# Kernel tuning notes

Hardware: AMD Instinct MI355X
Metric: run time of the kernel (lower is better)

## Reference

```python
import jax, jax.numpy as jnp
import numpy as np

B, L, C, V = 16, 600, 256, 256
OUT_SEQ = 6000
KSZ = 5
DILATIONS = (1, 2, 4)
N_BLOCKS = 10
COND = 256  # speaker(128) + noise(128)
TEMP = 10.0
EPS = 1e-5


def _ccbn(x, cond, gw, gb, bw, bb):
    # x: (B, C, L); conditional batch-norm: per-channel stats over (batch, length),
    # gamma/beta predicted from condition vector.
    mu = jnp.mean(x, axis=(0, 2), keepdims=True)
    var = jnp.var(x, axis=(0, 2), keepdims=True)
    xn = (x - mu) * jax.lax.rsqrt(var + EPS)
    gamma = 1.0 + cond @ gw + gb  # (B, C)
    beta = cond @ bw + bb         # (B, C)
    return xn * gamma[:, :, None] + beta[:, :, None]


def _conv1d(x, w, b, dil=1):
    # x: (B, C_in, L); w: (C_out, C_in, K)
    y = jax.lax.conv_general_dilated(
        x, w, window_strides=(1,), padding='SAME', rhs_dilation=(dil,),
        dimension_numbers=('NCH', 'OIH', 'NCH'))
    return y + b[None, :, None]


def setup_inputs() -> dict:
    key = jax.random.key(0)
    ks = jax.random.split(key, 20)
    s = 0.02
    inp = {
        'inputs': jax.random.randint(ks[0], (B, L), 0, V),
        'speaker_embeddings': jax.random.normal(ks[1], (B, 128), jnp.float32),
        'noise': jax.random.normal(ks[2], (B, 128), jnp.float32),
        'emb': jax.random.normal(ks[3], (V, C), jnp.float32) * s,
        # 10 blocks x 3 dilated convs
        'conv_w': jax.random.normal(ks[4], (N_BLOCKS, 3, C, C, KSZ), jnp.float32) * s,
        'conv_b': jnp.zeros((N_BLOCKS, 3, C), jnp.float32),
        # CCBN projections per conv (gamma/beta from condition)
        'g_w': jax.random.normal(ks[5], (N_BLOCKS, 3, COND, C), jnp.float32) * s,
        'g_b': jnp.zeros((N_BLOCKS, 3, C), jnp.float32),
        'b_w': jax.random.normal(ks[6], (N_BLOCKS, 3, COND, C), jnp.float32) * s,
        'b_b': jnp.zeros((N_BLOCKS, 3, C), jnp.float32),
        # TokenLength head: 2 CCBNs + conv1 (256->256,k1) + conv2 (256->1,k1)
        'tl_g_w': jax.random.normal(ks[7], (2, COND, C), jnp.float32) * s,
        'tl_g_b': jnp.zeros((2, C), jnp.float32),
        'tl_b_w': jax.random.normal(ks[8], (2, COND, C), jnp.float32) * s,
        'tl_b_b': jnp.zeros((2, C), jnp.float32),
        'tl_conv1_w': jax.random.normal(ks[9], (C, C, 1), jnp.float32) * s,
        'tl_conv1_b': jnp.zeros((C,), jnp.float32),
        'tl_conv2_w': jax.random.normal(ks[10], (1, C, 1), jnp.float32) * s,
        'tl_conv2_b': jnp.zeros((1,), jnp.float32),
    }
    return inp


def reference(inputs, speaker_embeddings, noise, emb, conv_w, conv_b,
              g_w, g_b, b_w, b_b, tl_g_w, tl_g_b, tl_b_w, tl_b_b,
              tl_conv1_w, tl_conv1_b, tl_conv2_w, tl_conv2_b):
    cond = jnp.concatenate([speaker_embeddings, noise], axis=-1)  # (B, COND)
    x = emb[inputs]                    # (B, L, C)
    x = jnp.transpose(x, (0, 2, 1))    # (B, C, L)

    # 10 unaligned blocks: residual stacks of CCBN -> ReLU -> dilated conv
    for blk in range(N_BLOCKS):
        y = x
        for j, d in enumerate(DILATIONS):
            y = jax.nn.relu(_ccbn(y, cond, g_w[blk, j], g_b[blk, j], b_w[blk, j], b_b[blk, j]))
            y = _conv1d(y, conv_w[blk, j], conv_b[blk, j], dil=d)
        x = x + y
    unaligned = x  # (B, C, L)

    # TokenLength head
    t = jax.nn.relu(_ccbn(unaligned, cond, tl_g_w[0], tl_g_b[0], tl_b_w[0], tl_b_b[0]))
    t = _conv1d(t, tl_conv1_w, tl_conv1_b)
    t = jax.nn.relu(_ccbn(t, cond, tl_g_w[1], tl_g_b[1], tl_b_w[1], tl_b_b[1]))
    t = _conv1d(t, tl_conv2_w, tl_conv2_b)  # (B, 1, L)
    token_lengths = jax.nn.relu(t[:, 0, :])  # (B, L)

    token_ends = jnp.cumsum(token_lengths, axis=-1)        # (B, L)
    token_centers = token_ends - token_lengths / 2.0        # (B, L)
    aligned_lengths = token_ends

    out_pos = jnp.arange(OUT_SEQ, dtype=jnp.float32)         # (OUT,)
    diff = token_centers[:, None, :] - out_pos[None, :, None]  # (B, OUT, L)
    logits = -(diff * diff) / TEMP
    weights = jax.nn.softmax(logits, axis=-1)                # (B, OUT, L)

    feats = jnp.transpose(unaligned, (0, 2, 1))              # (B, L, C)
    aligned_features = jnp.einsum('bol,blc->boc', weights, feats)  # (B, OUT, C)
    return aligned_features, aligned_lengths
```

## Files before the change

### kernel.cpp

```cpp
#include <hip/hip_runtime.h>
#include <math.h>

#define EPSv 1e-5f

typedef short short8 __attribute__((ext_vector_type(8)));
typedef float floatx4 __attribute__((ext_vector_type(4)));

__device__ __forceinline__ unsigned short f2bf(float x) {
  unsigned u = __float_as_uint(x);
  unsigned r = (u + 0x7fffu + ((u >> 16) & 1u)) >> 16;
  return (unsigned short)r;
}

__global__ void k_zero(float* __restrict__ p) {
  p[blockIdx.x * 256 + threadIdx.x] = 0.f;
}

__global__ void k_gamma_beta(const float* __restrict__ spk, const float* __restrict__ noise,
                             const float* __restrict__ g_w, const float* __restrict__ g_b,
                             const float* __restrict__ b_w, const float* __restrict__ b_b,
                             const float* __restrict__ tl_g_w, const float* __restrict__ tl_g_b,
                             const float* __restrict__ tl_b_w, const float* __restrict__ tl_b_b,
                             float* __restrict__ gammas, float* __restrict__ betas) {
  __shared__ float condl[16*256];
  int t = threadIdx.x;
  for (int idx = t; idx < 4096; idx += 256) {
    int b = idx >> 8, k = idx & 255;
    condl[idx] = (k < 128) ? spk[b*128 + k] : noise[b*128 + k - 128];
  }
  __syncthreads();
  int i = blockIdx.x;
  const float *gw, *bw, *gbias, *bbias;
  if (i < 30) { gw = g_w + (size_t)i*65536; bw = b_w + (size_t)i*65536; gbias = g_b + i*256; bbias = b_b + i*256; }
  else { int j = i - 30; gw = tl_g_w + (size_t)j*65536; bw = tl_b_w + (size_t)j*65536; gbias = tl_g_b + j*256; bbias = tl_b_b + j*256; }
  int co = (t & 63) + blockIdx.y * 64;
  int slot = t >> 6;
  float g[4] = {0.f,0.f,0.f,0.f}, bt[4] = {0.f,0.f,0.f,0.f};
  for (int k = 0; k < 256; ++k) {
    float gwv = gw[k*256 + co];
    float bwv = bw[k*256 + co];
    #pragma unroll
    for (int bb = 0; bb < 4; ++bb) {
      float cv = condl[(slot*4 + bb)*256 + k];
      g[bb]  = fmaf(cv, gwv, g[bb]);
      bt[bb] = fmaf(cv, bwv, bt[bb]);
    }
  }
  #pragma unroll
  for (int bb = 0; bb < 4; ++bb) {
    int b = slot*4 + bb;
    gammas[i*4096 + b*256 + co] = 1.0f + g[bb] + gbias[co];
    betas [i*4096 + b*256 + co] = bt[bb] + bbias[co];
  }
}

template<int TAPS>
__device__ __forceinline__ void wprep_body(const float* __restrict__ src,
                                           unsigned short* __restrict__ dst,
                                           int cotile, int chunk, int t) {
  int cow = t >> 2, ci8 = (t & 3) * 8;
  const float* s0 = src + ((size_t)(cotile*64 + cow)*256 + chunk*32 + ci8)*TAPS;
  float v[8*TAPS];
  #pragma unroll
  for (int i = 0; i < 8*TAPS; ++i) v[i] = s0[i];
  unsigned short* dblk = dst + (size_t)cotile*(8*TAPS*4096) + (size_t)chunk*(TAPS*4096);
  #pragma unroll
  for (int tap = 0; tap < TAPS; ++tap) {
    unsigned hi2[4], lo2[4];
    #pragma unroll
    for (int jj = 0; jj < 4; ++jj) {
      float a = v[(jj*2+0)*TAPS + tap], b = v[(jj*2+1)*TAPS + tap];
      unsigned short ha = f2bf(a), hb = f2bf(b);
      unsigned short la = f2bf(a - __uint_as_float((unsigned)ha << 16));
      unsigned short lb = f2bf(b - __uint_as_float((unsigned)hb << 16));
      hi2[jj] = (unsigned)ha | ((unsigned)hb << 16);
      lo2[jj] = (unsigned)la | ((unsigned)lb << 16);
    }
    uint4 H; H.x = hi2[0]; H.y = hi2[1]; H.z = hi2[2]; H.w = hi2[3];
    uint4 L; L.x = lo2[0]; L.y = lo2[1]; L.z = lo2[2]; L.w = lo2[3];
    *(uint4*)(dblk + (size_t)(tap*2)*2048 + cow*32 + ci8) = H;
    *(uint4*)(dblk + (size_t)(tap*2+1)*2048 + cow*32 + ci8) = L;
  }
}

__global__ __launch_bounds__(256) void k_wprep(const float* __restrict__ conv_w,
                                               const float* __restrict__ tl_c1_w,
                                               unsigned short* __restrict__ wp) {
  int cc = blockIdx.x;
  int cotile = blockIdx.y >> 3, chunk = blockIdx.y & 7;
  if (cc == 30) wprep_body<1>(tl_c1_w, wp + (size_t)30*655360, cotile, chunk, threadIdx.x);
  else          wprep_body<5>(conv_w + (size_t)cc*327680, wp + (size_t)cc*655360, cotile, chunk, threadIdx.x);
}

__global__ void k_embed2(const int* __restrict__ inp, const float* __restrict__ emb,
                         float* __restrict__ x, float* __restrict__ stat0) {
  int bx = blockIdx.x;
  int c = threadIdx.x;
  int r0 = bx * 60;
  float s = 0.f, s2 = 0.f;
  for (int r = 0; r < 60; ++r) {
    int row = inp[r0 + r];
    float v = emb[(size_t)row*256 + c];
    x[(size_t)(r0 + r)*256 + c] = v;
    s += v; s2 = fmaf(v, v, s2);
  }
  atomicAdd(&stat0[c], s);
  atomicAdd(&stat0[256 + c], s2);
}

template<int TAPS>
__global__ __launch_bounds__(256) void k_convm(const float* __restrict__ zin, float* __restrict__ out,
                        const float* __restrict__ stat_in, float* __restrict__ stat_out,
                        const float* __restrict__ gam, const float* __restrict__ bet,
                        const unsigned short* __restrict__ wpc,
                        const float* __restrict__ bias, int dil, int mode) {
  __shared__ unsigned short Zhi[80*40];
  __shared__ unsigned short Zlo[80*40];
  __shared__ float s_sc[256];
  __shared__ float s_sh[256];
  __shared__ float lsum[64];
  __shared__ float lsq[64];
  int t = threadIdx.x;
  int bx = blockIdx.x;
  int b  = bx / 10;
  int l0 = (bx % 10) * 64;
  int co0 = blockIdx.y * 64;
  int PAD = ((TAPS - 1)/2) * dil;
  int ROWS = 64 + 2*PAD;
  int w = t >> 6, lane = t & 63;
  int lsub = (w & 1) * 32, cosub = (w >> 1) * 32;
  int quad = lane >> 4, nlan = lane & 15;
  if (t < 64) { lsum[t] = 0.f; lsq[t] = 0.f; }
  {
    float s = stat_in[t], s2 = stat_in[256 + t];
    float mu = s * (1.0f/9600.0f);
    float var = s2 * (1.0f/9600.0f) - mu*mu;
    float rs = rsqrtf(var + EPSv);
    float scale = rs * gam[b*256 + t];
    s_sc[t] = scale;
    s_sh[t] = fmaf(-mu, scale, bet[b*256 + t]);
  }

  floatx4 acc[2][2];
  #pragma unroll
  for (int i = 0; i < 2; ++i)
    #pragma unroll
    for (int j = 0; j < 2; ++j) acc[i][j] = (floatx4){0.f,0.f,0.f,0.f};

  const float* zb = zin + (size_t)b*600*256;
  int srow = t >> 3, fq = t & 7;
  int ar0 = (lsub + nlan) * 40 + quad * 8;
  int ar1 = (lsub + 16 + nlan) * 40 + quad * 8;

  for (int chunk = 0; chunk < 8; ++chunk) {
    int ci0 = chunk * 32;
    const unsigned short* pch = wpc + (size_t)(blockIdx.y*8 + chunk) * (TAPS*4096);
    short8 bh[TAPS][2], bl[TAPS][2];
    #pragma unroll
    for (int tap = 0; tap < TAPS; ++tap) {
      #pragma unroll
      for (int nt = 0; nt < 2; ++nt) {
        int cw = (cosub + nt*16 + nlan)*32 + quad*8;
        bh[tap][nt] = *(const short8*)(pch + (size_t)(tap*2)*2048 + cw);
        bl[tap][nt] = *(const short8*)(pch + (size_t)(tap*2+1)*2048 + cw);
      }
    }
    __syncthreads();
    float4 sc4 = *(const float4*)&s_sc[ci0 + fq*4];
    float4 sh4 = *(const float4*)&s_sh[ci0 + fq*4];
    for (int r = srow; r < ROWS; r += 32) {
      int gl = l0 - PAD + r;
      bool inr = (gl >= 0 && gl < 600);
      float4 z = {0,0,0,0};
      if (inr) z = *(const float4*)&zb[(size_t)gl*256 + ci0 + fq*4];
      float v0 = inr ? fmaxf(fmaf(z.x, sc4.x, sh4.x), 0.f) : 0.f;
      float v1 = inr ? fmaxf(fmaf(z.y, sc4.y, sh4.y), 0.f) : 0.f;
      float v2 = inr ? fmaxf(fmaf(z.z, sc4.z, sh4.z), 0.f) : 0.f;
      float v3 = inr ? fmaxf(fmaf(z.w, sc4.w, sh4.w), 0.f) : 0.f;
      unsigned short h0 = f2bf(v0), h1 = f2bf(v1), h2 = f2bf(v2), h3 = f2bf(v3);
      unsigned short e0 = f2bf(v0 - __uint_as_float((unsigned)h0 << 16));
      unsigned short e1 = f2bf(v1 - __uint_as_float((unsigned)h1 << 16));
      unsigned short e2 = f2bf(v2 - __uint_as_float((unsigned)h2 << 16));
      unsigned short e3 = f2bf(v3 - __uint_as_float((unsigned)h3 << 16));
      uint2 vh; vh.x = (unsigned)h0 | ((unsigned)h1 << 16);
      vh.y = (unsigned)h2 | ((unsigned)h3 << 16);
      uint2 vl; vl.x = (unsigned)e0 | ((unsigned)e1 << 16);
      vl.y = (unsigned)e2 | ((unsigned)e3 << 16);
      *(uint2*)&Zhi[r*40 + fq*4] = vh;
      *(uint2*)&Zlo[r*40 + fq*4] = vl;
    }
    __syncthreads();
    #pragma unroll
    for (int tap = 0; tap < TAPS; ++tap) {
      int sh = tap * dil * 40;
      short8 ah0 = *(const short8*)&Zhi[ar0 + sh];
      short8 ah1 = *(const short8*)&Zhi[ar1 + sh];
      short8 al0 = *(const short8*)&Zlo[ar0 + sh];
      short8 al1 = *(const short8*)&Zlo[ar1 + sh];
      #pragma unroll
      for (int nt = 0; nt < 2; ++nt) {
        acc[0][nt] = __builtin_amdgcn_mfma_f32_16x16x32_bf16(ah0, bh[tap][nt], acc[0][nt], 0, 0, 0);
        acc[0][nt] = __builtin_amdgcn_mfma_f32_16x16x32_bf16(ah0, bl[tap][nt], acc[0][nt], 0, 0, 0);
        acc[0][nt] = __builtin_amdgcn_mfma_f32_16x16x32_bf16(al0, bh[tap][nt], acc[0][nt], 0, 0, 0);
        acc[1][nt] = __builtin_amdgcn_mfma_f32_16x16x32_bf16(ah1, bh[tap][nt], acc[1][nt], 0, 0, 0);
        acc[1][nt] = __builtin_amdgcn_mfma_f32_16x16x32_bf16(ah1, bl[tap][nt], acc[1][nt], 0, 0, 0);
        acc[1][nt] = __builtin_amdgcn_mfma_f32_16x16x32_bf16(al1, bh[tap][nt], acc[1][nt], 0, 0, 0);
      }
    }
  }

  float bsv[2], ssum[2] = {0.f, 0.f}, ssq[2] = {0.f, 0.f};
  #pragma unroll
  for (int nt = 0; nt < 2; ++nt) bsv[nt] = bias[co0 + cosub + nt*16 + nlan];
  #pragma unroll
  for (int mt = 0; mt < 2; ++mt) {
    #pragma unroll
    for (int r = 0; r < 4; ++r) {
      int l = l0 + lsub + mt*16 + quad*4 + r;
      if (l < 600) {
        size_t rowo = ((size_t)(b*600 + l))*256 + co0 + cosub;
        #pragma unroll
        for (int nt = 0; nt < 2; ++nt) {
          float v = acc[mt][nt][r] + bsv[nt];
          float* dst = &out[rowo + nt*16 + nlan];
          if (mode) v += *dst;
          *dst = v;
          ssum[nt] += v;
          ssq[nt] = fmaf(v, v, ssq[nt]);
        }
      }
    }
  }
  #pragma unroll
  for (int nt = 0; nt < 2; ++nt) {
    ssum[nt] += __shfl_xor(ssum[nt], 16, 64);
    ssum[nt] += __shfl_xor(ssum[nt], 32, 64);
    ssq[nt]  += __shfl_xor(ssq[nt], 16, 64);
    ssq[nt]  += __shfl_xor(ssq[nt], 32, 64);
  }
  if (quad == 0) {
    #pragma unroll
    for (int nt = 0; nt < 2; ++nt) {
      atomicAdd(&lsum[cosub + nt*16 + nlan], ssum[nt]);
      atomicAdd(&lsq [cosub + nt*16 + nlan], ssq[nt]);
    }
  }
  __syncthreads();
  if (t < 64) {
    atomicAdd(&stat_out[co0 + t], lsum[t]);
    atomicAdd(&stat_out[256 + co0 + t], lsq[t]);
  }
}

__global__ void k_tl2(const float* __restrict__ z, const float* __restrict__ stat,
                      const float* __restrict__ gam, const float* __restrict__ bet,
                      const float* __restrict__ w2, const float* __restrict__ b2,
                      float* __restrict__ tl) {
  int t = threadIdx.x;
  int row = blockIdx.x * 4 + (t >> 6);
  int lane = t & 63;
  int b = row / 600;
  float4 s1 = *(const float4*)&stat[lane*4];
  float4 s2 = *(const float4*)&stat[256 + lane*4];
  float4 gm = *(const float4*)&gam[b*256 + lane*4];
  float4 bt = *(const float4*)&bet[b*256 + lane*4];
  float sc[4], sh[4];
  {
    float sv[4] = {s1.x, s1.y, s1.z, s1.w};
    float qv[4] = {s2.x, s2.y, s2.z, s2.w};
    float gv[4] = {gm.x, gm.y, gm.z, gm.w};
    float bv[4] = {bt.x, bt.y, bt.z, bt.w};
    #pragma unroll
    for (int i = 0; i < 4; ++i) {
      float mu = sv[i] * (1.0f/9600.0f);
      float var = qv[i] * (1.0f/9600.0f) - mu*mu;
      float rs = rsqrtf(var + EPSv);
      sc[i] = rs * gv[i];
      sh[i] = fmaf(-mu, sc[i], bv[i]);
    }
  }
  float4 zr = *(const float4*)&z[(size_t)row*256 + lane*4];
  float4 wr = *(const float4*)&w2[lane*4];
  float z0 = fmaxf(fmaf(zr.x, sc[0], sh[0]), 0.f);
  float z1 = fmaxf(fmaf(zr.y, sc[1], sh[1]), 0.f);
  float z2 = fmaxf(fmaf(zr.z, sc[2], sh[2]), 0.f);
  float z3 = fmaxf(fmaf(zr.w, sc[3], sh[3]), 0.f);
  float s = z0*wr.x + z1*wr.y + z2*wr.z + z3*wr.w;
  for (int m = 32; m >= 1; m >>= 1) s += __shfl_xor(s, m, 64);
  if (lane == 0) tl[row] = fmaxf(s + b2[0], 0.f);
}

__global__ void k_cumsum(const float* __restrict__ tl, float* __restrict__ centers,
                         float* __restrict__ out_len) {
  int b = blockIdx.x; int lane = threadIdx.x;
  float carry = 0.f;
  for (int ch = 0; ch < 10; ++ch) {
    int l = ch*64 + lane;
    float v = (l < 600) ? tl[b*600 + l] : 0.f;
    float s = v;
    #pragma unroll
    for (int off = 1; off < 64; off <<= 1) {
      float n = __shfl_up(s, off, 64);
      if (lane >= off) s += n;
    }
    float ends = carry + s;
    if (l < 600) {
      centers[b*600 + l] = ends - 0.5f*v;
      out_len[b*600 + l] = ends;
    }
    carry = __shfl(ends, 63, 64);
  }
}

__global__ void k_tobf16(const float* __restrict__ x, unsigned short* __restrict__ fbT) {
  __shared__ unsigned short T[64*66];
  int b = blockIdx.x, lt = blockIdx.y, ct = blockIdx.z;
  int t = threadIdx.x;
  int i4 = t >> 6;
  int j = t & 63;
  #pragma unroll
  for (int r = 0; r < 16; ++r) {
    int li = i4*16 + r;
    int l = lt*64 + li;
    float v = (l < 600) ? x[((size_t)(b*600 + l))*256 + ct*64 + j] : 0.f;
    T[j*66 + li] = f2bf(v);
  }
  __syncthreads();
  int row = t >> 2, seg = (t & 3) * 16;
  unsigned vv[8];
  #pragma unroll
  for (int k = 0; k < 8; ++k)
    vv[k] = *(const unsigned*)&T[row*66 + seg + k*2];
  size_t dsth = ((size_t)(b*256 + ct*64 + row))*640 + lt*64 + seg;
  unsigned* du = (unsigned*)fbT;
  uint4 a; a.x = vv[0]; a.y = vv[1]; a.z = vv[2]; a.w = vv[3];
  uint4 c4; c4.x = vv[4]; c4.y = vv[5]; c4.z = vv[6]; c4.w = vv[7];
  *(uint4*)(du + dsth/2) = a;
  *(uint4*)(du + dsth/2 + 4) = c4;
}

__global__ __launch_bounds__(256) void k_align2(const unsigned short* __restrict__ fbT,
                        const float* __restrict__ centers, float* __restrict__ outp) {
  __shared__ float cen[600];
  __shared__ float mrow[64];
  __shared__ float isum[64];
  __shared__ unsigned short Wt[64*72];
  __shared__ unsigned short Ft[256*72];
  int b = blockIdx.x;
  int o0 = blockIdx.y * 64;
  int t = threadIdx.x;
  int wv = t >> 6, lane = t & 63;
  for (int i = t; i < 600; i += 256) cen[i] = centers[b*600 + i];
  __syncthreads();
  for (int rr = 0; rr < 16; ++rr) {
    int oi = wv*16 + rr;
    float opos = (float)(o0 + oi);
    float mx = -3.0e38f;
    for (int l = lane; l < 600; l += 64) {
      float d = cen[l] - opos;
      mx = fmaxf(mx, -d*d*0.1f);
    }
    #pragma unroll
    for (int mm = 32; mm >= 1; mm >>= 1) mx = fmaxf(mx, __shfl_xor(mx, mm, 64));
    float sum = 0.f;
    for (int l = lane; l < 600; l += 64) {
      float d = cen[l] - opos;
      sum += __expf(-d*d*0.1f - mx);
    }
    #pragma unroll
    for (int mm = 32; mm >= 1; mm >>= 1) sum += __shfl_xor(sum, mm, 64);
    if (lane == 0) { mrow[oi] = mx; isum[oi] = 1.0f / sum; }
  }
  __syncthreads();
  floatx4 acc[4][4];
  #pragma unroll
  for (int i = 0; i < 4; ++i)
    #pragma unroll
    for (int j = 0; j < 4; ++j)
      acc[i][j] = (floatx4){0.f, 0.f, 0.f, 0.f};
  int quad = lane >> 4;
  int nlan = lane & 15;
  int oi_w = t >> 2;
  int lq = (t & 3) * 16;
  float mo = mrow[oi_w];
  float opos_w = (float)(o0 + oi_w);
  const unsigned short* srcb = fbT + ((size_t)b*256)*640;

  for (int ch = 0; ch < 10; ++ch) {
    int lc0 = ch * 64;
    __syncthreads();
    #pragma unroll
    for (int jj = 0; jj < 16; jj += 2) {
      int l0i = lc0 + lq + jj;
      float e0 = 0.f, e1 = 0.f;
      if (l0i < 600)     { float d = cen[l0i] - opos_w;     e0 = __expf(-d*d*0.1f - mo); }
      if (l0i + 1 < 600) { float d = cen[l0i + 1] - opos_w; e1 = __expf(-d*d*0.1f - mo); }
      unsigned pk = (unsigned)f2bf(e0) | ((unsigned)f2bf(e1) << 16);
      *(unsigned*)&Wt[oi_w*72 + lq + jj] = pk;
    }
    #pragma unroll
    for (int it = 0; it < 8; ++it) {
      int idx = t + it*256;
      int c = idx >> 3, part = idx & 7;
      uint4 v = *(const uint4*)(srcb + (size_t)c*640 + lc0 + part*8);
      *(uint4*)&Ft[c*72 + part*8] = v;
    }
    __syncthreads();
    #pragma unroll
    for (int ks = 0; ks < 2; ++ks) {
      int ko = ks*32 + quad*8;
      short8 af[4], bfr[4];
      #pragma unroll
      for (int mt = 0; mt < 4; ++mt)
        af[mt] = *(const short8*)&Wt[(mt*16 + nlan)*72 + ko];
      #pragma unroll
      for (int nt = 0; nt < 4; ++nt)
        bfr[nt] = *(const short8*)&Ft[(wv*64 + nt*16 + nlan)*72 + ko];
      #pragma unroll
      for (int mt = 0; mt < 4; ++mt)
        #pragma unroll
        for (int nt = 0; nt < 4; ++nt)
          acc[mt][nt] = __builtin_amdgcn_mfma_f32_16x16x32_bf16(af[mt], bfr[nt], acc[mt][nt], 0, 0, 0);
    }
  }
  #pragma unroll
  for (int mt = 0; mt < 4; ++mt) {
    #pragma unroll
    for (int r = 0; r < 4; ++r) {
      int oi = mt*16 + quad*4 + r;
      int o = o0 + oi;
      if (o < 6000) {
        float sc = isum[oi];
        #pragma unroll
        for (int nt = 0; nt < 4; ++nt) {
          int c = wv*64 + nt*16 + nlan;
          outp[((size_t)b*6000 + o)*256 + c] = acc[mt][nt][r] * sc;
        }
      }
    }
  }
}

extern "C" void kernel_launch(void* const* d_in, const int* in_sizes, int n_in,
                              void* d_out, int out_size, void* d_ws, size_t ws_size,
                              hipStream_t stream) {
  const int*   inputs = (const int*)  d_in[0];
  const float* spk    = (const float*)d_in[1];
  const float* noise  = (const float*)d_in[2];
  const float* emb    = (const float*)d_in[3];
  const float* conv_w = (const float*)d_in[4];
  const float* conv_b = (const float*)d_in[5];
  const float* g_w    = (const float*)d_in[6];
  const float* g_b    = (const float*)d_in[7];
  const float* b_w    = (const float*)d_in[8];
  const float* b_b    = (const float*)d_in[9];
  const float* tl_g_w = (const float*)d_in[10];
  const float* tl_g_b = (const float*)d_in[11];
  const float* tl_b_w = (const float*)d_in[12];
  const float* tl_b_b = (const float*)d_in[13];
  const float* tl_c1_w = (const float*)d_in[14];
  const float* tl_c1_b = (const float*)d_in[15];
  const float* tl_c2_w = (const float*)d_in[16];
  const float* tl_c2_b = (const float*)d_in[17];
  float* out = (float*)d_out;

  float* ws = (float*)d_ws;
  float* x       = ws;
  float* A       = x + 2457600;
  float* Bf      = A + 2457600;
  float* gammas  = Bf + 2457600;
  float* betas   = gammas + 131072;
  float* statacc = betas + 131072;
  float* tl      = statacc + 16384;
  float* cen     = tl + 9600;
  unsigned short* wp = (unsigned short*)(cen + 9600);
  unsigned short* fbT = (unsigned short*)Bf;

  k_zero<<<dim3(64), dim3(256), 0, stream>>>(statacc);
  k_wprep<<<dim3(31, 32), dim3(256), 0, stream>>>(conv_w, tl_c1_w, wp);
  k_gamma_beta<<<dim3(32, 4), dim3(256), 0, stream>>>(spk, noise, g_w, g_b, b_w, b_b,
      tl_g_w, tl_g_b, tl_b_w, tl_b_b, gammas, betas);
  k_embed2<<<dim3(160), dim3(256), 0, stream>>>(inputs, emb, x, statacc);

  const int dils[3] = {1, 2, 4};
  for (int blk = 0; blk < 10; ++blk) {
    const float* srcs[3] = {x, A, Bf};
    float*       dsts[3] = {A, Bf, x};
    for (int j = 0; j < 3; ++j) {
      int idx = blk*3 + j;
      int mode = (j == 2) ? 1 : 0;
      k_convm<5><<<dim3(160, 4), dim3(256), 0, stream>>>(srcs[j], dsts[j],
          statacc + idx*512, statacc + (idx+1)*512,
          gammas + idx*4096, betas + idx*4096,
          wp + (size_t)idx*655360, conv_b + idx*256, dils[j], mode);
    }
  }
  k_convm<1><<<dim3(160, 4), dim3(256), 0, stream>>>(x, A,
      statacc + 30*512, statacc + 31*512,
      gammas + 30*4096, betas + 30*4096,
      wp + (size_t)30*655360, tl_c1_b, 1, 0);
  k_tl2<<<dim3(2400), dim3(256), 0, stream>>>(A, statacc + 31*512,
      gammas + 31*4096, betas + 31*4096, tl_c2_w, tl_c2_b, tl);
  k_cumsum<<<dim3(16), dim3(64), 0, stream>>>(tl, cen, out + 24576000);
  k_tobf16<<<dim3(16, 10, 4), dim3(256), 0, stream>>>(x, fbT);
  k_align2<<<dim3(16, 94), dim3(256), 0, stream>>>(fbT, cen, out);
}
```

Baseline: 1.714 ms.

## Double-buffer conv input staging and fuse softmax sum into weight generation

The dilated conv kernel now keeps two LDS buffers for the transformed input chunk. It prefetches global loads two chunks ahead and transforms the next chunk while the current one feeds MFMA, which removes one barrier per chunk. The alignment kernel drops the separate exp pass used for the softmax denominator and accumulates it while building the bf16 weight tile. Weight-tile writes become 16-byte vector stores. This trades extra registers and LDS, which may lower occupancy, for fewer exp evaluations and more load/compute overlap.

```diff
diff --git a/kernel.cpp b/kernel.cpp
--- a/kernel.cpp
+++ b/kernel.cpp
@@ -114,8 +114,8 @@
                         const float* __restrict__ gam, const float* __restrict__ bet,
                         const unsigned short* __restrict__ wpc,
                         const float* __restrict__ bias, int dil, int mode) {
-  __shared__ unsigned short Zhi[80*40];
-  __shared__ unsigned short Zlo[80*40];
+  __shared__ unsigned short Zhi[2][3200];
+  __shared__ unsigned short Zlo[2][3200];
   __shared__ float s_sc[256];
   __shared__ float s_sh[256];
   __shared__ float lsum[64];
@@ -152,9 +152,64 @@
   int ar0 = (lsub + nlan) * 40 + quad * 8;
   int ar1 = (lsub + 16 + nlan) * 40 + quad * 8;
 
-  for (int chunk = 0; chunk < 8; ++chunk) {
+  bool va[3]; long zbase[3];
+  #pragma unroll
+  for (int i = 0; i < 3; ++i) {
+    int r = srow + i*32;
+    int gl = l0 - PAD + r;
+    va[i] = (r < ROWS) && (gl >= 0) && (gl < 600);
+    zbase[i] = (long)gl*256 + fq*4;
+  }
+  float4 pz[2][3];
+
+  auto prefetch = [&](int chunk) {
+    int set = chunk & 1;
+    #pragma unroll
+    for (int i = 0; i < 3; ++i) {
+      float4 z = {0.f,0.f,0.f,0.f};
+      if (va[i]) z = *(const float4*)&zb[zbase[i] + chunk*32];
+      pz[set][i] = z;
+    }
+  };
+  auto transform = [&](int chunk) {
+    int p = chunk & 1;
     int ci0 = chunk * 32;
-    const unsigned short* pch = wpc + (size_t)(blockIdx.y*8 + chunk) * (TAPS*4096);
+    float4 sc4 = *(const float4*)&s_sc[ci0 + fq*4];
+    float4 sh4 = *(const float4*)&s_sh[ci0 + fq*4];
+    #pragma unroll
+    for (int i = 0; i < 3; ++i) {
+      int r = srow + i*32;
+      if (r < ROWS) {
+        float4 z = pz[p][i];
+        bool inr = va[i];
+        float v0 = inr ? fmaxf(fmaf(z.x, sc4.x, sh4.x), 0.f) : 0.f;
+        float v1 = inr ? fmaxf(fmaf(z.y, sc4.y, sh4.y), 0.f) : 0.f;
+        float v2 = inr ? fmaxf(fmaf(z.z, sc4.z, sh4.z), 0.f) : 0.f;
+        float v3 = inr ? fmaxf(fmaf(z.w, sc4.w, sh4.w), 0.f) : 0.f;
+        unsigned short h0 = f2bf(v0), h1 = f2bf(v1), h2 = f2bf(v2), h3 = f2bf(v3);
+        unsigned short e0 = f2bf(v0 - __uint_as_float((unsigned)h0 << 16));
+        unsigned short e1 = f2bf(v1 - __uint_as_float((unsigned)h1 << 16));
+        unsigned short e2 = f2bf(v2 - __uint_as_float((unsigned)h2 << 16));
+        unsigned short e3 = f2bf(v3 - __uint_as_float((unsigned)h3 << 16));
+        uint2 vh; vh.x = (unsigned)h0 | ((unsigned)h1 << 16);
+        vh.y = (unsigned)h2 | ((unsigned)h3 << 16);
+        uint2 vl; vl.x = (unsigned)e0 | ((unsigned)e1 << 16);
+        vl.y = (unsigned)e2 | ((unsigned)e3 << 16);
+        *(uint2*)&Zhi[p][r*40 + fq*4] = vh;
+        *(uint2*)&Zlo[p][r*40 + fq*4] = vl;
+      }
+    }
+  };
+
+  prefetch(0);
+  prefetch(1);
+  __syncthreads();
+  transform(0);
+
+  for (int c = 0; c < 8; ++c) {
+    int p = c & 1;
+    __syncthreads();
+    const unsigned short* pch = wpc + (size_t)(blockIdx.y*8 + c) * (TAPS*4096);
     short8 bh[TAPS][2], bl[TAPS][2];
     #pragma unroll
     for (int tap = 0; tap < TAPS; ++tap) {
@@ -165,38 +220,15 @@
         bl[tap][nt] = *(const short8*)(pch + (size_t)(tap*2+1)*2048 + cw);
       }
     }
-    __syncthreads();
-    float4 sc4 = *(const float4*)&s_sc[ci0 + fq*4];
-    float4 sh4 = *(const float4*)&s_sh[ci0 + fq*4];
-    for (int r = srow; r < ROWS; r += 32) {
-      int gl = l0 - PAD + r;
-      bool inr = (gl >= 0 && gl < 600);
-      float4 z = {0,0,0,0};
-      if (inr) z = *(const float4*)&zb[(size_t)gl*256 + ci0 + fq*4];
-      float v0 = inr ? fmaxf(fmaf(z.x, sc4.x, sh4.x), 0.f) : 0.f;
-      float v1 = inr ? fmaxf(fmaf(z.y, sc4.y, sh4.y), 0.f) : 0.f;
-      float v2 = inr ? fmaxf(fmaf(z.z, sc4.z, sh4.z), 0.f) : 0.f;
-      float v3 = inr ? fmaxf(fmaf(z.w, sc4.w, sh4.w), 0.f) : 0.f;
-      unsigned short h0 = f2bf(v0), h1 = f2bf(v1), h2 = f2bf(v2), h3 = f2bf(v3);
-      unsigned short e0 = f2bf(v0 - __uint_as_float((unsigned)h0 << 16));
-      unsigned short e1 = f2bf(v1 - __uint_as_float((unsigned)h1 << 16));
-      unsigned short e2 = f2bf(v2 - __uint_as_float((unsigned)h2 << 16));
-      unsigned short e3 = f2bf(v3 - __uint_as_float((unsigned)h3 << 16));
-      uint2 vh; vh.x = (unsigned)h0 | ((unsigned)h1 << 16);
-      vh.y = (unsigned)h2 | ((unsigned)h3 << 16);
-      uint2 vl; vl.x = (unsigned)e0 | ((unsigned)e1 << 16);
-      vl.y = (unsigned)e2 | ((unsigned)e3 << 16);
-      *(uint2*)&Zhi[r*40 + fq*4] = vh;
-      *(uint2*)&Zlo[r*40 + fq*4] = vl;
-    }
-    __syncthreads();
+    if (c < 6) prefetch(c + 2);
+    if (c < 7) transform(c + 1);
     #pragma unroll
     for (int tap = 0; tap < TAPS; ++tap) {
       int sh = tap * dil * 40;
-      short8 ah0 = *(const short8*)&Zhi[ar0 + sh];
-      short8 ah1 = *(const short8*)&Zhi[ar1 + sh];
-      short8 al0 = *(const short8*)&Zlo[ar0 + sh];
-      short8 al1 = *(const short8*)&Zlo[ar1 + sh];
+      short8 ah0 = *(const short8*)&Zhi[p][ar0 + sh];
+      short8 ah1 = *(const short8*)&Zhi[p][ar1 + sh];
+      short8 al0 = *(const short8*)&Zlo[p][ar0 + sh];
+      short8 al1 = *(const short8*)&Zlo[p][ar1 + sh];
       #pragma unroll
       for (int nt = 0; nt < 2; ++nt) {
         acc[0][nt] = __builtin_amdgcn_mfma_f32_16x16x32_bf16(ah0, bh[tap][nt], acc[0][nt], 0, 0, 0);
@@ -362,14 +394,7 @@
     }
     #pragma unroll
     for (int mm = 32; mm >= 1; mm >>= 1) mx = fmaxf(mx, __shfl_xor(mx, mm, 64));
-    float sum = 0.f;
-    for (int l = lane; l < 600; l += 64) {
-      float d = cen[l] - opos;
-      sum += __expf(-d*d*0.1f - mx);
-    }
-    #pragma unroll
-    for (int mm = 32; mm >= 1; mm >>= 1) sum += __shfl_xor(sum, mm, 64);
-    if (lane == 0) { mrow[oi] = mx; isum[oi] = 1.0f / sum; }
+    if (lane == 0) mrow[oi] = mx;
   }
   __syncthreads();
   floatx4 acc[4][4];
@@ -381,22 +406,30 @@
   int quad = lane >> 4;
   int nlan = lane & 15;
   int oi_w = t >> 2;
-  int lq = (t & 3) * 16;
+  int sbase = t & 3;
   float mo = mrow[oi_w];
   float opos_w = (float)(o0 + oi_w);
+  float psum = 0.f;
   const unsigned short* srcb = fbT + ((size_t)b*256)*640;
 
   for (int ch = 0; ch < 10; ++ch) {
     int lc0 = ch * 64;
     __syncthreads();
     #pragma unroll
-    for (int jj = 0; jj < 16; jj += 2) {
-      int l0i = lc0 + lq + jj;
-      float e0 = 0.f, e1 = 0.f;
-      if (l0i < 600)     { float d = cen[l0i] - opos_w;     e0 = __expf(-d*d*0.1f - mo); }
-      if (l0i + 1 < 600) { float d = cen[l0i + 1] - opos_w; e1 = __expf(-d*d*0.1f - mo); }
-      unsigned pk = (unsigned)f2bf(e0) | ((unsigned)f2bf(e1) << 16);
-      *(unsigned*)&Wt[oi_w*72 + lq + jj] = pk;
+    for (int sidx = 0; sidx < 2; ++sidx) {
+      int seg = sbase + sidx*4;
+      unsigned pk[4];
+      #pragma unroll
+      for (int jj = 0; jj < 8; jj += 2) {
+        int li = lc0 + seg*8 + jj;
+        float e0 = 0.f, e1 = 0.f;
+        if (li < 600)     { float d = cen[li] - opos_w;     e0 = __expf(-d*d*0.1f - mo); }
+        if (li + 1 < 600) { float d = cen[li + 1] - opos_w; e1 = __expf(-d*d*0.1f - mo); }
+        psum += e0 + e1;
+        pk[jj>>1] = (unsigned)f2bf(e0) | ((unsigned)f2bf(e1) << 16);
+      }
+      uint4 v; v.x = pk[0]; v.y = pk[1]; v.z = pk[2]; v.w = pk[3];
+      *(uint4*)&Wt[oi_w*72 + seg*8] = v;
     }
     #pragma unroll
     for (int it = 0; it < 8; ++it) {
@@ -423,6 +456,10 @@
           acc[mt][nt] = __builtin_amdgcn_mfma_f32_16x16x32_bf16(af[mt], bfr[nt], acc[mt][nt], 0, 0, 0);
     }
   }
+  psum += __shfl_xor(psum, 1, 64);
+  psum += __shfl_xor(psum, 2, 64);
+  if ((t & 3) == 0) isum[oi_w] = 1.0f / psum;
+  __syncthreads();
   #pragma unroll
   for (int mt = 0; mt < 4; ++mt) {
     #pragma unroll
```

New measurement: 1.962 ms. 1.15x slower.
